# Kernel optimization log

Measured on AMD Instinct MI355X. Metric: run time of the kernel, lower is better.

The kernel has to match this reference:

```python
import jax, jax.numpy as jnp
import numpy as np

N, K, D = 1_048_576, 16, 8
EPS = 1e-6


def setup_inputs() -> dict:
    key = jax.random.key(0)
    k1, k2, k3, k4 = jax.random.split(key, 4)
    x = jax.random.normal(k1, (N, D), dtype=jnp.float32)
    means = jax.random.normal(k2, (K, D), dtype=jnp.float32)
    # near-identity Cholesky factors so L @ L.T is well conditioned
    chol_var = jnp.broadcast_to(jnp.eye(D, dtype=jnp.float32), (K, D, D)) \
        + 0.05 * jax.random.normal(k3, (K, D, D), dtype=jnp.float32)
    pi = jnp.ones((K,), dtype=jnp.float32) / K \
        + 0.1 * jax.random.uniform(k4, (K,), dtype=jnp.float32)
    return {"x": x, "means": means, "chol_var": chol_var, "pi": pi}


def reference(x, means, chol_var, pi):
    d = x.shape[-1]
    # per-component covariance: tril(L) @ tril(L)^T + eps*I  -> [K, D, D]
    Ltri = jnp.tril(chol_var)
    cov = jnp.einsum('kij,klj->kil', Ltri, Ltri) + EPS * jnp.eye(d, dtype=x.dtype)
    # MultivariateNormal(mean, cov).log_prob == Cholesky of cov + triangular solve
    L = jnp.linalg.cholesky(cov)                                 # [K, D, D]
    diff = x[:, None, :] - means[None, :, :]                     # [N, K, D]
    b = jnp.transpose(diff, (1, 2, 0))                           # [K, D, N]
    y = jax.scipy.linalg.solve_triangular(L, b, lower=True)      # [K, D, N]
    quad = jnp.sum(y * y, axis=1)                                # [K, N]
    half_logdet = jnp.sum(jnp.log(jnp.diagonal(L, axis1=-2, axis2=-1)), axis=-1)  # [K]
    log2pi = jnp.log(jnp.asarray(2.0 * np.pi, dtype=x.dtype))
    log_probs = -0.5 * (quad + d * log2pi) - half_logdet[:, None]  # [K, N]
    # mixture weights via log_softmax, stable logsumexp over components
    weighted = log_probs.T + jax.nn.log_softmax(pi)              # [N, K]
    return jax.nn.logsumexp(weighted, axis=1)                    # [N]
```

## Files before the change

kernel.cpp:

```cpp
#include <hip/hip_runtime.h>
#include <hip/hip_bf16.h>
#include <math.h>

#define KCOMP 16
#define DDIM 8
#define CSTRIDE 48
#define PPT 8

__global__ __launch_bounds__(256) void gmm_fused(const float* __restrict__ x,
                                                 const float* __restrict__ means,
                                                 const float* __restrict__ chol_var,
                                                 const float* __restrict__ pi,
                                                 float* __restrict__ out, int n) {
    __shared__ float sc[KCOMP * CSTRIDE];

    const int k = threadIdx.x;
    if (k < KCOMP) {
        float Lc[DDIM][DDIM];
#pragma unroll
        for (int i = 0; i < DDIM; ++i)
#pragma unroll
            for (int j = 0; j < DDIM; ++j)
                Lc[i][j] = (j <= i) ? chol_var[k * DDIM * DDIM + i * DDIM + j] : 0.0f;

        float C[DDIM][DDIM];
#pragma unroll
        for (int i = 0; i < DDIM; ++i)
#pragma unroll
            for (int j = 0; j <= i; ++j) {
                float s = 0.0f;
#pragma unroll
                for (int m = 0; m < DDIM; ++m) s += Lc[i][m] * Lc[j][m];
                C[i][j] = s;
            }
#pragma unroll
        for (int i = 0; i < DDIM; ++i) C[i][i] += 1e-6f;

        float L[DDIM][DDIM];
#pragma unroll
        for (int j = 0; j < DDIM; ++j) {
            float d = C[j][j];
#pragma unroll
            for (int m = 0; m < DDIM; ++m) if (m < j) d -= L[j][m] * L[j][m];
            float ljj = sqrtf(d);
            L[j][j] = ljj;
            float inv = 1.0f / ljj;
#pragma unroll
            for (int i = 0; i < DDIM; ++i) {
                if (i <= j) continue;
                float s = C[i][j];
#pragma unroll
                for (int m = 0; m < DDIM; ++m) if (m < j) s -= L[i][m] * L[j][m];
                L[i][j] = s * inv;
            }
        }

        float Li[DDIM][DDIM];
#pragma unroll
        for (int i = 0; i < DDIM; ++i)
#pragma unroll
            for (int j = 0; j < DDIM; ++j) Li[i][j] = 0.0f;
#pragma unroll
        for (int c = 0; c < DDIM; ++c) {
            Li[c][c] = 1.0f / L[c][c];
#pragma unroll
            for (int i = 0; i < DDIM; ++i) {
                if (i <= c) continue;
                float s = 0.0f;
#pragma unroll
                for (int m = 0; m < DDIM; ++m)
                    if (m >= c && m < i) s += L[i][m] * Li[m][c];
                Li[i][c] = -s / L[i][i];
            }
        }

        float hld = 0.0f;
#pragma unroll
        for (int i = 0; i < DDIM; ++i) hld += __logf(L[i][i]);

        float mx = pi[0];
#pragma unroll
        for (int j = 1; j < KCOMP; ++j) mx = fmaxf(mx, pi[j]);
        float ssum = 0.0f;
#pragma unroll
        for (int j = 0; j < KCOMP; ++j) ssum += __expf(pi[j] - mx);
        float lse = mx + __logf(ssum);

        const float LOG2PI = 1.83787706640934548356f;
        float constk = (pi[k] - lse) - hld - 0.5f * (float)DDIM * LOG2PI;

        const float r = 0.70710678118654752440f;
        float* c = sc + k * CSTRIDE;
        int idx = 0;
#pragma unroll
        for (int i = 0; i < DDIM; ++i)
#pragma unroll
            for (int j = 0; j < DDIM; ++j)
                if (j <= i) c[idx++] = Li[i][j] * r;
#pragma unroll
        for (int i = 0; i < DDIM; ++i) {
            float b = 0.0f;
#pragma unroll
            for (int j = 0; j < DDIM; ++j)
                if (j <= i) b += Li[i][j] * means[k * DDIM + j];
            c[36 + i] = -b * r;
        }
        c[44] = constk;
        c[45] = 0.0f; c[46] = 0.0f; c[47] = 0.0f;
    }
    __syncthreads();

    float Cmax = sc[44];
#pragma unroll
    for (int j = 1; j < KCOMP; ++j) Cmax = fmaxf(Cmax, sc[j * CSTRIDE + 44]);

    const int base = blockIdx.x * (256 * PPT) + threadIdx.x;
    float xv[PPT][DDIM];
#pragma unroll
    for (int p = 0; p < PPT; ++p) {
        int pt = base + p * 256;
        const float4* xp = (const float4*)(x + (size_t)pt * DDIM);
        float4 a = xp[0];
        float4 b = xp[1];
        xv[p][0] = a.x; xv[p][1] = a.y; xv[p][2] = a.z; xv[p][3] = a.w;
        xv[p][4] = b.x; xv[p][5] = b.y; xv[p][6] = b.z; xv[p][7] = b.w;
    }

    float s[PPT];
#pragma unroll
    for (int p = 0; p < PPT; ++p) s[p] = 0.0f;

#pragma unroll 1
    for (int kk = 0; kk < KCOMP; ++kk) {
        const float4* c4 = (const float4*)(sc + kk * CSTRIDE);
        float cc[48];
#pragma unroll
        for (int t = 0; t < 12; ++t) {
            float4 v = c4[t];
            cc[4 * t + 0] = v.x; cc[4 * t + 1] = v.y;
            cc[4 * t + 2] = v.z; cc[4 * t + 3] = v.w;
        }
        const float ck = cc[44] - Cmax;
#pragma unroll
        for (int p = 0; p < PPT; ++p) {
            float q = 0.0f;
            int idx = 0;
#pragma unroll
            for (int i = 0; i < DDIM; ++i) {
                float y = cc[36 + i];
#pragma unroll
                for (int j = 0; j <= i; ++j) { y = fmaf(cc[idx], xv[p][j], y); ++idx; }
                q = fmaf(y, y, q);
            }
            s[p] += __expf(ck - q);
        }
    }

#pragma unroll
    for (int p = 0; p < PPT; ++p) {
        int pt = base + p * 256;
        if (pt < n) out[pt] = Cmax + __logf(s[p]);
    }
}

extern "C" void kernel_launch(void* const* d_in, const int* in_sizes, int n_in,
                              void* d_out, int out_size, void* d_ws, size_t ws_size,
                              hipStream_t stream) {
    const float* x        = (const float*)d_in[0];
    const float* means    = (const float*)d_in[1];
    const float* chol_var = (const float*)d_in[2];
    const float* pi       = (const float*)d_in[3];
    float* out = (float*)d_out;

    int n = in_sizes[0] / DDIM;
    int nthreads = (n + PPT - 1) / PPT;
    gmm_fused<<<(nthreads + 255) / 256, 256, 0, stream>>>(x, means, chol_var, pi, out, n);
}
```

Baseline: 98.62 us.

## Split per-component setup into a separate one-block kernel and shrink points per thread

Before, every block redid the Cholesky factorisation, triangular inverse and log-softmax for all 16 components. Now a single small setup kernel does this once, writes a coefficient table to a global device array, and folds the max-constant subtraction into that table. The evaluation kernel copies the table into shared memory and processes 4 points per thread instead of 8, with a launch bound hint for higher occupancy. The cost is a second kernel launch and a serial dependency between the two kernels.

Result: no change. 97.88 us, median of 2 (-0.8%).

```diff
diff --git a/kernel.cpp b/kernel.cpp
--- a/kernel.cpp
+++ b/kernel.cpp
@@ -1,19 +1,17 @@
 #include <hip/hip_runtime.h>
-#include <hip/hip_bf16.h>
 #include <math.h>
 
 #define KCOMP 16
 #define DDIM 8
 #define CSTRIDE 48
-#define PPT 8
+#define PPT 4
 
-__global__ __launch_bounds__(256) void gmm_fused(const float* __restrict__ x,
-                                                 const float* __restrict__ means,
-                                                 const float* __restrict__ chol_var,
-                                                 const float* __restrict__ pi,
-                                                 float* __restrict__ out, int n) {
-    __shared__ float sc[KCOMP * CSTRIDE];
+__device__ float g_tab[KCOMP * CSTRIDE];
 
+__global__ __launch_bounds__(64) void gmm_setup(const float* __restrict__ means,
+                                                const float* __restrict__ chol_var,
+                                                const float* __restrict__ pi) {
+    __shared__ float sconst[KCOMP];
     const int k = threadIdx.x;
     if (k < KCOMP) {
         float Lc[DDIM][DDIM];
@@ -90,7 +88,7 @@
         float constk = (pi[k] - lse) - hld - 0.5f * (float)DDIM * LOG2PI;
 
         const float r = 0.70710678118654752440f;
-        float* c = sc + k * CSTRIDE;
+        float* c = g_tab + k * CSTRIDE;
         int idx = 0;
 #pragma unroll
         for (int i = 0; i < DDIM; ++i)
@@ -105,14 +103,33 @@
                 if (j <= i) b += Li[i][j] * means[k * DDIM + j];
             c[36 + i] = -b * r;
         }
-        c[44] = constk;
-        c[45] = 0.0f; c[46] = 0.0f; c[47] = 0.0f;
+        sconst[k] = constk;
+    }
+    __syncthreads();
+    if (k < KCOMP) {
+        float Cmax = sconst[0];
+#pragma unroll
+        for (int j = 1; j < KCOMP; ++j) Cmax = fmaxf(Cmax, sconst[j]);
+        float* c = g_tab + k * CSTRIDE;
+        c[44] = sconst[k] - Cmax;
+        c[45] = Cmax;
+        c[46] = 0.0f;
+        c[47] = 0.0f;
+    }
+}
+
+__global__ __launch_bounds__(256, 4) void gmm_eval(const float* __restrict__ x,
+                                                   float* __restrict__ out, int n) {
+    __shared__ float sc[KCOMP * CSTRIDE];
+
+    {
+        const int t = threadIdx.x;
+        if (t < (KCOMP * CSTRIDE) / 4)
+            ((float4*)sc)[t] = ((const float4*)g_tab)[t];
     }
     __syncthreads();
 
-    float Cmax = sc[44];
-#pragma unroll
-    for (int j = 1; j < KCOMP; ++j) Cmax = fmaxf(Cmax, sc[j * CSTRIDE + 44]);
+    const float Cmax = sc[45];
 
     const int base = blockIdx.x * (256 * PPT) + threadIdx.x;
     float xv[PPT][DDIM];
@@ -140,7 +157,7 @@
             cc[4 * t + 0] = v.x; cc[4 * t + 1] = v.y;
             cc[4 * t + 2] = v.z; cc[4 * t + 3] = v.w;
         }
-        const float ck = cc[44] - Cmax;
+        const float ck = cc[44];
 #pragma unroll
         for (int p = 0; p < PPT; ++p) {
             float q = 0.0f;
@@ -171,8 +188,12 @@
     const float* chol_var = (const float*)d_in[2];
     const float* pi       = (const float*)d_in[3];
     float* out = (float*)d_out;
+    (void)d_ws; (void)ws_size;
 
     int n = in_sizes[0] / DDIM;
+
+    gmm_setup<<<1, 64, 0, stream>>>(means, chol_var, pi);
+
     int nthreads = (n + PPT - 1) / PPT;
-    gmm_fused<<<(nthreads + 255) / 256, 256, 0, stream>>>(x, means, chol_var, pi, out, n);
+    gmm_eval<<<(nthreads + 255) / 256, 256, 0, stream>>>(x, out, n);
 }
```
